# Kernel tuning notes

Hardware: AMD Instinct MI355X
Metric: run time of the kernel (lower is better)

The kernel has to match this reference:

```python
import jax, jax.numpy as jnp
import numpy as np

DEPTH = 6
INPUT_DIM = 512
HIDDEN = [128, 64]
OUT_DIM = 8
BATCH = 8192
NUM_LEAVES = 2 ** DEPTH            # 64
NUM_INTERNAL = 2 ** DEPTH - 1      # 63 routing Dense(1, sigmoid) nodes


def setup_inputs() -> dict:
    key = jax.random.key(0)
    ks = jax.random.split(key, 9)
    s = lambda fan_in: 1.0 / np.sqrt(fan_in)
    return {
        "x": jax.random.normal(ks[0], (BATCH, INPUT_DIM), dtype=jnp.float32),
        # routers: one Dense(input_dim -> 1) per internal node
        "router_W": jax.random.normal(ks[1], (NUM_INTERNAL, INPUT_DIM), dtype=jnp.float32) * s(INPUT_DIM),
        "router_b": jnp.zeros((NUM_INTERNAL,), dtype=jnp.float32),
        # leaf MLPs: Dense(512->128, relu) -> Dense(128->64, relu) -> Dense(64->8, linear), one per leaf
        "W1": jax.random.normal(ks[2], (NUM_LEAVES, INPUT_DIM, HIDDEN[0]), dtype=jnp.float32) * s(INPUT_DIM),
        "b1": jnp.zeros((NUM_LEAVES, HIDDEN[0]), dtype=jnp.float32),
        "W2": jax.random.normal(ks[3], (NUM_LEAVES, HIDDEN[0], HIDDEN[1]), dtype=jnp.float32) * s(HIDDEN[0]),
        "b2": jnp.zeros((NUM_LEAVES, HIDDEN[1]), dtype=jnp.float32),
        "W3": jax.random.normal(ks[4], (NUM_LEAVES, HIDDEN[1], OUT_DIM), dtype=jnp.float32) * s(HIDDEN[1]),
        "b3": jnp.zeros((NUM_LEAVES, OUT_DIM), dtype=jnp.float32),
    }


def reference(x, router_W, router_b, W1, b1, W2, b2, W3, b3):
    B = x.shape[0]
    depth = int(np.log2(router_W.shape[0] + 1))
    # All routing probabilities in one fused GEMM: [B, num_internal]
    route = jax.nn.sigmoid(jnp.einsum('bi,ni->bn', x, router_W) + router_b)
    # Soft routing down the tree: interleave left/right child probabilities per level.
    p = jnp.ones((B, 1), dtype=x.dtype)
    offset = 0
    for level in range(depth):  # small fixed loop over tree levels
        n = 2 ** level
        d = route[:, offset:offset + n]              # P(go left) at each node in level
        p = jnp.stack([p * d, p * (1.0 - d)], axis=-1).reshape(B, 2 * n)
        offset += n
    # p: [B, num_leaves] leaf arrival probabilities (sums to 1 per row)
    # Leaf experts as batched (grouped) GEMMs over the leaf axis l.
    h = jax.nn.relu(jnp.einsum('bi,lih->blh', x, W1) + b1)   # [B, L, 128]
    h = jax.nn.relu(jnp.einsum('blh,lhk->blk', h, W2) + b2)  # [B, L, 64]
    pred = jnp.einsum('blk,lko->blo', h, W3) + b3            # [B, L, out] (linear output act)
    # Weighted mixture over leaves.
    return jnp.einsum('bl,blo->bo', p, pred)                 # [B, out]
```

## Files before the change

### kernel.cpp

```cpp
#include <hip/hip_runtime.h>
#include <hip/hip_bf16.h>


typedef _Float16 f16;
typedef _Float16 f16x8 __attribute__((ext_vector_type(8)));
typedef float    f32x4 __attribute__((ext_vector_type(4)));
typedef float    f32x16 __attribute__((ext_vector_type(16)));

#define MFMA16(a,b,c) __builtin_amdgcn_mfma_f32_16x16x32_f16((a),(b),(c),0,0,0)
#define MFMA32(a,b,c) __builtin_amdgcn_mfma_f32_32x32x16_f16((a),(b),(c),0,0,0)

typedef const __attribute__((address_space(1))) void gv_t;
typedef __attribute__((address_space(3))) void lv_t;
__device__ __forceinline__ void cp16(const void* g, char* lds_dst) {
  __builtin_amdgcn_global_load_lds((gv_t*)g, (lv_t*)lds_dst, 16, 0, 0);
}

#define WS_XH    0u
#define WS_W1F   8388608u
#define WS_W2F   16777216u
#define WS_W3F   17825792u
#define WS_RWF   17956864u
#define WS_NEED  18022400u

#define L_X   0
#define L_H1  32768
#define L_H2  50176
#define L_P   59392
#define L_TOT 63488

__global__ __launch_bounds__(256) void prep_all(
    const float* __restrict__ x, const float* __restrict__ rW,
    const float* __restrict__ W1, const float* __restrict__ W2,
    const float* __restrict__ W3,
    f16* __restrict__ xh, f16* __restrict__ w1f, f16* __restrict__ w2f,
    f16* __restrict__ w3f, f16* __restrict__ rwf, float* __restrict__ out) {
  const int bid = blockIdx.x, t = threadIdx.x;
  if (bid < 512) {
    const int l = bid >> 3, kc = bid & 7;
    const int lane = t & 63;
#pragma unroll
    for (int p = 0; p < 4; ++p) {
      int c = p * 4 + (t >> 6);
      int ng = c >> 2, ksl = c & 3;
      int n = ng * 32 + (lane & 31);
      int k0 = kc * 64 + ksl * 16 + (lane >> 5) * 8;
      const float* src = W1 + ((size_t)l * 512 + k0) * 128 + n;
      f16x8 h;
#pragma unroll
      for (int j = 0; j < 8; ++j) h[j] = (f16)src[(size_t)j * 128];
      *(f16x8*)(w1f + ((size_t)((l * 4 + ng) * 32 + kc * 4 + ksl) * 64 + lane) * 8) = h;
    }
  } else if (bid < 768) {
    size_t base = (size_t)(bid - 512) * 16384;
#pragma unroll
    for (int i = 0; i < 8; ++i) {
      size_t idx = base + ((size_t)t + i * 256) * 8;
      float4 a = *(const float4*)(x + idx);
      float4 b = *(const float4*)(x + idx + 4);
      f16x8 h = {(f16)a.x,(f16)a.y,(f16)a.z,(f16)a.w,(f16)b.x,(f16)b.y,(f16)b.z,(f16)b.w};
      *(f16x8*)(xh + idx) = h;
    }
  } else if (bid < 832) {
    const int l = bid - 768;
    const int lane = t & 63;
#pragma unroll
    for (int p = 0; p < 4; ++p) {
      int c = p * 4 + (t >> 6);
      int nb = c >> 2, ks = c & 3;
      int n = nb * 16 + (lane & 15);
      int k0 = ks * 32 + (lane >> 4) * 8;
      const float* src = W2 + (size_t)l * 8192 + (size_t)k0 * 64 + n;
      f16x8 h;
#pragma unroll
      for (int j = 0; j < 8; ++j) h[j] = (f16)src[(size_t)j * 64];
      *(f16x8*)(w2f + ((size_t)((l * 4 + nb) * 4 + ks) * 64 + lane) * 8) = h;
    }
    if (t < 128) {
      int ks = t >> 6, lane2 = t & 63;
      int n = lane2 & 15;
      int k0 = ks * 32 + (lane2 >> 4) * 8;
      f16x8 h;
#pragma unroll
      for (int j = 0; j < 8; ++j)
        h[j] = (n < 8) ? (f16)W3[((size_t)l * 64 + k0 + j) * 8 + n] : (f16)0.f;
      *(f16x8*)(w3f + ((size_t)(l * 2 + ks) * 64 + lane2) * 8) = h;
    }
  } else {
    int c = (bid - 832) * 4 + (t >> 6);
    int ngr = c >> 5, ks = c & 31;
    int lane = t & 63;
    int n = ngr * 32 + (lane & 31);
    int k0 = ks * 16 + (lane >> 5) * 8;
    f16x8 h;
#pragma unroll
    for (int j = 0; j < 8; ++j)
      h[j] = (n < 63) ? (f16)rW[(size_t)n * 512 + k0 + j] : (f16)0.f;
    *(f16x8*)(rwf + ((size_t)c * 64 + lane) * 8) = h;
    size_t o0 = ((size_t)(bid - 832) * 256 + t) * 16;
    float4 z = {0.f, 0.f, 0.f, 0.f};
#pragma unroll
    for (int i = 0; i < 4; ++i) *(float4*)(out + o0 + i * 4) = z;
  }
}

__global__ __launch_bounds__(256, 2) void fused_tree(
    const f16* __restrict__ xh, const f16* __restrict__ w1f,
    const f16* __restrict__ w2f, const f16* __restrict__ w3f,
    const f16* __restrict__ rwf, const float* __restrict__ rb,
    const float* __restrict__ b1, const float* __restrict__ b2,
    const float* __restrict__ b3, float* __restrict__ out) {
  __shared__ char smem[L_TOT];
  f16*   x_lds   = (f16*)(smem + L_X);
  f16*   h1_lds  = (f16*)(smem + L_H1);
  float* route_s = (float*)(smem + L_H1);
  f16*   h2_lds  = (f16*)(smem + L_H2);
  float* p_lds   = (float*)(smem + L_P);

  const int t = threadIdx.x;
  const int w = t >> 6, L = t & 63;
  const int l16 = L & 15, quad = L >> 4;
  const int r31 = L & 31, kp = L >> 5;

  const int bid = blockIdx.x;
  const int r8 = bid & 7;
  const int lg0 = (r8 >> 1) * 16;
  const int btp = (bid >> 3) * 2 + (r8 & 1);
  const int b0 = btp * 64;

#pragma unroll
  for (int j = 0; j < 8; ++j) {
    int r = w * 8 + j;
    int u = (L & 56) | ((L & 7) ^ (r & 7));
    cp16(xh + (size_t)(b0 + 32 + r) * 512 + u * 8, smem + r * 1024);
  }
  f16x8 a0[32];
#pragma unroll
  for (int ks = 0; ks < 32; ++ks)
    a0[ks] = *(const f16x8*)(xh + (size_t)(b0 + r31) * 512 + ks * 16 + kp * 8);
  __syncthreads();

  {
    const int btr = w >> 1, ngr = w & 1;
    f32x16 accr;
#pragma unroll
    for (int i = 0; i < 16; ++i) accr[i] = 0.f;
    const f16* rbase = rwf + (size_t)(ngr * 32) * 512 + (size_t)L * 8;
#pragma unroll
    for (int ks = 0; ks < 32; ++ks) {
      f16x8 B = *(const f16x8*)(rbase + (size_t)ks * 512);
      f16x8 A;
      if (btr == 0) A = a0[ks];
      else {
        int u = ks * 2 + kp;
        A = *(const f16x8*)(x_lds + r31 * 512 + ((u & 56) | ((u & 7) ^ (r31 & 7))) * 8);
      }
      accr = MFMA32(A, B, accr);
    }
    int node = ngr * 32 + r31;
    float rbv = (node < 63) ? rb[node] : 0.f;
#pragma unroll
    for (int reg = 0; reg < 16; ++reg) {
      int rr = btr * 32 + (reg & 3) + 8 * (reg >> 2) + 4 * kp;
      route_s[rr * 68 + node] = 1.f / (1.f + __expf(-(accr[reg] + rbv)));
    }
  }
  __syncthreads();
  {
    int row = t >> 2, j0 = t & 3;
#pragma unroll
    for (int i = 0; i < 4; ++i) {
      int l = lg0 + j0 * 4 + i;
      float pr = 1.f;
#pragma unroll
      for (int lev = 0; lev < 6; ++lev) {
        int node = (1 << lev) - 1 + (l >> (6 - lev));
        float d = route_s[row * 68 + node];
        pr *= ((l >> (5 - lev)) & 1) ? (1.f - d) : d;
      }
      p_lds[row * 16 + j0 * 4 + i] = pr;
    }
  }
  __syncthreads();

  const f16* w1base = w1f + ((size_t)(lg0 * 4 + w) * 32) * 512 + (size_t)L * 8;
  f16x8 bq[2][4];
#pragma unroll
  for (int s = 0; s < 4; ++s) bq[0][s] = *(const f16x8*)(w1base + (size_t)s * 512);

  f32x4 acc_out = {0.f, 0.f, 0.f, 0.f};
  const int mt = w >> 1, nt2 = w & 1;
  const int n1 = w * 32 + r31;

#pragma unroll 1
  for (int li = 0; li < 16; ++li) {
    const int l = lg0 + li;
    const size_t leafoff = (size_t)li * 65536;

    f32x16 acc1r, acc1l;
#pragma unroll
    for (int i = 0; i < 16; ++i) { acc1r[i] = 0.f; acc1l[i] = 0.f; }

#pragma unroll
    for (int q = 0; q < 8; ++q) {
      f16x8 A1[4];
#pragma unroll
      for (int s = 0; s < 4; ++s) {
        int u = (q * 4 + s) * 2 + kp;
        A1[s] = *(const f16x8*)(x_lds + r31 * 512 + ((u & 56) | ((u & 7) ^ (r31 & 7))) * 8);
      }
      size_t nxt = (q < 7) ? (leafoff + (size_t)(q + 1) * 2048)
                           : ((li < 15) ? (leafoff + 65536) : (leafoff + 7 * 2048));
#pragma unroll
      for (int s = 0; s < 4; ++s)
        bq[(q + 1) & 1][s] = *(const f16x8*)(w1base + nxt + (size_t)s * 512);
      __builtin_amdgcn_s_setprio(1);
#pragma unroll
      for (int s = 0; s < 4; ++s)
        acc1r = MFMA32(a0[q * 4 + s], bq[q & 1][s], acc1r);
#pragma unroll
      for (int s = 0; s < 4; ++s)
        acc1l = MFMA32(A1[s], bq[q & 1][s], acc1l);
      __builtin_amdgcn_s_setprio(0);
    }

    f16x8 bw2[2][4];
#pragma unroll
    for (int n16 = 0; n16 < 2; ++n16)
#pragma unroll
      for (int ks = 0; ks < 4; ++ks)
        bw2[n16][ks] = *(const f16x8*)(w2f + ((size_t)((l * 4 + nt2 * 2 + n16) * 4 + ks) * 64 + L) * 8);
    f16x8 bw3[2];
#pragma unroll
    for (int ks = 0; ks < 2; ++ks)
      bw3[ks] = *(const f16x8*)(w3f + ((size_t)(l * 2 + ks) * 64 + L) * 8);

    const float bias1 = b1[l * 128 + n1];

#pragma unroll
    for (int reg = 0; reg < 16; ++reg) {
      int rr = (reg & 3) + 8 * (reg >> 2) + 4 * kp;
      float v0 = acc1r[reg] + bias1;
      float v1 = acc1l[reg] + bias1;
      h1_lds[rr * 136 + n1] = (f16)(v0 > 0.f ? v0 : 0.f);
      h1_lds[(rr + 32) * 136 + n1] = (f16)(v1 > 0.f ? v1 : 0.f);
    }
    __syncthreads();

#define GEMM2_BT(btv)                                                          \
    {                                                                          \
      f32x4 acc2[2] = {{0.f,0.f,0.f,0.f},{0.f,0.f,0.f,0.f}};                   \
      _Pragma("unroll")                                                        \
      for (int ks = 0; ks < 4; ++ks) {                                         \
        f16x8 A = *(const f16x8*)(h1_lds + ((btv) * 32 + mt * 16 + l16) * 136 + ks * 32 + quad * 8); \
        _Pragma("unroll")                                                      \
        for (int n16 = 0; n16 < 2; ++n16) acc2[n16] = MFMA16(A, bw2[n16][ks], acc2[n16]); \
      }                                                                        \
      _Pragma("unroll")                                                        \
      for (int n16 = 0; n16 < 2; ++n16) {                                      \
        int n2 = nt2 * 32 + n16 * 16 + l16;                                    \
        float bias2 = b2[l * 64 + n2];                                         \
        _Pragma("unroll")                                                      \
        for (int rg = 0; rg < 4; ++rg) {                                       \
          int r2 = mt * 16 + quad * 4 + rg;                                    \
          float v = acc2[n16][rg] + bias2;                                     \
          v = v > 0.f ? v : 0.f;                                               \
          h2_lds[((btv) * 32 + r2) * 72 + n2] = (f16)(v * p_lds[((btv) * 32 + r2) * 16 + li]); \
        }                                                                      \
      }                                                                        \
    }

    GEMM2_BT(0)
    GEMM2_BT(1)
#undef GEMM2_BT
    __syncthreads();

#pragma unroll
    for (int ks = 0; ks < 2; ++ks) {
      f16x8 A = *(const f16x8*)(h2_lds + (w * 16 + l16) * 72 + ks * 32 + quad * 8);
      acc_out = MFMA16(A, bw3[ks], acc_out);
    }
  }

  if (l16 < 8) {
    float b3v[16];
#pragma unroll
    for (int li2 = 0; li2 < 16; ++li2) b3v[li2] = b3[(lg0 + li2) * 8 + l16];
#pragma unroll
    for (int rg = 0; rg < 4; ++rg) {
      int rloc = w * 16 + quad * 4 + rg;
      float v = acc_out[rg];
#pragma unroll
      for (int li2 = 0; li2 < 16; ++li2) v += p_lds[rloc * 16 + li2] * b3v[li2];
      atomicAdd(out + (size_t)(b0 + rloc) * 8 + l16, v);
    }
  }
}

extern "C" void kernel_launch(void* const* d_in, const int* in_sizes, int n_in,
                              void* d_out, int out_size, void* d_ws, size_t ws_size,
                              hipStream_t stream) {
  const float* x  = (const float*)d_in[0];
  const float* rW = (const float*)d_in[1];
  const float* rb = (const float*)d_in[2];
  const float* W1 = (const float*)d_in[3];
  const float* b1 = (const float*)d_in[4];
  const float* W2 = (const float*)d_in[5];
  const float* b2 = (const float*)d_in[6];
  const float* W3 = (const float*)d_in[7];
  const float* b3 = (const float*)d_in[8];
  float* out = (float*)d_out;

  if (ws_size < WS_NEED) return;

  char* ws = (char*)d_ws;
  f16* xh  = (f16*)(ws + WS_XH);
  f16* w1f = (f16*)(ws + WS_W1F);
  f16* w2f = (f16*)(ws + WS_W2F);
  f16* w3f = (f16*)(ws + WS_W3F);
  f16* rwf = (f16*)(ws + WS_RWF);

  prep_all<<<848, 256, 0, stream>>>(x, rW, W1, W2, W3, xh, w1f, w2f, w3f, rwf, out);
  fused_tree<<<512, 256, 0, stream>>>(xh, w1f, w2f, w3f, rwf, rb, b1, b2, b3, out);
}
```

Before: 190.6 us.

## Halve batch tile to 32 rows per block, dropping x LDS staging

Each block now handles 32 batch rows instead of 64, so the second half of x no longer needs staging in LDS. The x-in-LDS path is removed, which cuts shared memory per block from about 62 KB to 15 KB. The grid doubles to 1024 blocks and launch bounds are raised to 4 blocks per CU for more parallelism and occupancy. The cost is that each W1/W2/W3 weight fetch is now reused over half as many rows, so weight traffic doubles, the output partials split across two waves, and there are twice as many atomics.

```diff
diff --git a/kernel.cpp b/kernel.cpp
--- a/kernel.cpp
+++ b/kernel.cpp
@@ -9,12 +9,6 @@
 
 #define MFMA16(a,b,c) __builtin_amdgcn_mfma_f32_16x16x32_f16((a),(b),(c),0,0,0)
 #define MFMA32(a,b,c) __builtin_amdgcn_mfma_f32_32x32x16_f16((a),(b),(c),0,0,0)
-
-typedef const __attribute__((address_space(1))) void gv_t;
-typedef __attribute__((address_space(3))) void lv_t;
-__device__ __forceinline__ void cp16(const void* g, char* lds_dst) {
-  __builtin_amdgcn_global_load_lds((gv_t*)g, (lv_t*)lds_dst, 16, 0, 0);
-}
 
 #define WS_XH    0u
 #define WS_W1F   8388608u
@@ -23,11 +17,10 @@
 #define WS_RWF   17956864u
 #define WS_NEED  18022400u
 
-#define L_X   0
-#define L_H1  32768
-#define L_H2  50176
-#define L_P   59392
-#define L_TOT 63488
+#define L_H1  0
+#define L_H2  8704
+#define L_P   13312
+#define L_TOT 15360
 
 __global__ __launch_bounds__(256) void prep_all(
     const float* __restrict__ x, const float* __restrict__ rW,
@@ -104,14 +97,13 @@
   }
 }
 
-__global__ __launch_bounds__(256, 2) void fused_tree(
+__global__ __launch_bounds__(256, 4) void fused_tree(
     const f16* __restrict__ xh, const f16* __restrict__ w1f,
     const f16* __restrict__ w2f, const f16* __restrict__ w3f,
     const f16* __restrict__ rwf, const float* __restrict__ rb,
     const float* __restrict__ b1, const float* __restrict__ b2,
     const float* __restrict__ b3, float* __restrict__ out) {
   __shared__ char smem[L_TOT];
-  f16*   x_lds   = (f16*)(smem + L_X);
   f16*   h1_lds  = (f16*)(smem + L_H1);
   float* route_s = (float*)(smem + L_H1);
   f16*   h2_lds  = (f16*)(smem + L_H2);
@@ -126,22 +118,15 @@
   const int r8 = bid & 7;
   const int lg0 = (r8 >> 1) * 16;
   const int btp = (bid >> 3) * 2 + (r8 & 1);
-  const int b0 = btp * 64;
-
-#pragma unroll
-  for (int j = 0; j < 8; ++j) {
-    int r = w * 8 + j;
-    int u = (L & 56) | ((L & 7) ^ (r & 7));
-    cp16(xh + (size_t)(b0 + 32 + r) * 512 + u * 8, smem + r * 1024);
-  }
+  const int b0 = btp * 32;
+
   f16x8 a0[32];
 #pragma unroll
   for (int ks = 0; ks < 32; ++ks)
     a0[ks] = *(const f16x8*)(xh + (size_t)(b0 + r31) * 512 + ks * 16 + kp * 8);
-  __syncthreads();
-
-  {
-    const int btr = w >> 1, ngr = w & 1;
+
+  if (w < 2) {
+    const int ngr = w;
     f32x16 accr;
 #pragma unroll
     for (int i = 0; i < 16; ++i) accr[i] = 0.f;
@@ -149,24 +134,18 @@
 #pragma unroll
     for (int ks = 0; ks < 32; ++ks) {
       f16x8 B = *(const f16x8*)(rbase + (size_t)ks * 512);
-      f16x8 A;
-      if (btr == 0) A = a0[ks];
-      else {
-        int u = ks * 2 + kp;
-        A = *(const f16x8*)(x_lds + r31 * 512 + ((u & 56) | ((u & 7) ^ (r31 & 7))) * 8);
-      }
-      accr = MFMA32(A, B, accr);
+      accr = MFMA32(a0[ks], B, accr);
     }
     int node = ngr * 32 + r31;
     float rbv = (node < 63) ? rb[node] : 0.f;
 #pragma unroll
     for (int reg = 0; reg < 16; ++reg) {
-      int rr = btr * 32 + (reg & 3) + 8 * (reg >> 2) + 4 * kp;
+      int rr = (reg & 3) + 8 * (reg >> 2) + 4 * kp;
       route_s[rr * 68 + node] = 1.f / (1.f + __expf(-(accr[reg] + rbv)));
     }
   }
   __syncthreads();
-  {
+  if (t < 128) {
     int row = t >> 2, j0 = t & 3;
 #pragma unroll
     for (int i = 0; i < 4; ++i) {
@@ -183,32 +162,28 @@
   }
   __syncthreads();
 
-  const f16* w1base = w1f + ((size_t)(lg0 * 4 + w) * 32) * 512 + (size_t)L * 8;
+  const int ng = w;
+  const f16* w1base = w1f + ((size_t)(lg0 * 4 + ng) * 32) * 512 + (size_t)L * 8;
   f16x8 bq[2][4];
 #pragma unroll
   for (int s = 0; s < 4; ++s) bq[0][s] = *(const f16x8*)(w1base + (size_t)s * 512);
 
   f32x4 acc_out = {0.f, 0.f, 0.f, 0.f};
   const int mt = w >> 1, nt2 = w & 1;
-  const int n1 = w * 32 + r31;
+  const int rb3 = w >> 1, ks3 = w & 1;
+  const int n1 = ng * 32 + r31;
 
 #pragma unroll 1
   for (int li = 0; li < 16; ++li) {
     const int l = lg0 + li;
     const size_t leafoff = (size_t)li * 65536;
 
-    f32x16 acc1r, acc1l;
-#pragma unroll
-    for (int i = 0; i < 16; ++i) { acc1r[i] = 0.f; acc1l[i] = 0.f; }
+    f32x16 acc1;
+#pragma unroll
+    for (int i = 0; i < 16; ++i) acc1[i] = 0.f;
 
 #pragma unroll
     for (int q = 0; q < 8; ++q) {
-      f16x8 A1[4];
-#pragma unroll
-      for (int s = 0; s < 4; ++s) {
-        int u = (q * 4 + s) * 2 + kp;
-        A1[s] = *(const f16x8*)(x_lds + r31 * 512 + ((u & 56) | ((u & 7) ^ (r31 & 7))) * 8);
-      }
       size_t nxt = (q < 7) ? (leafoff + (size_t)(q + 1) * 2048)
                            : ((li < 15) ? (leafoff + 65536) : (leafoff + 7 * 2048));
 #pragma unroll
@@ -217,10 +192,7 @@
       __builtin_amdgcn_s_setprio(1);
 #pragma unroll
       for (int s = 0; s < 4; ++s)
-        acc1r = MFMA32(a0[q * 4 + s], bq[q & 1][s], acc1r);
-#pragma unroll
-      for (int s = 0; s < 4; ++s)
-        acc1l = MFMA32(A1[s], bq[q & 1][s], acc1l);
+        acc1 = MFMA32(a0[q * 4 + s], bq[q & 1][s], acc1);
       __builtin_amdgcn_s_setprio(0);
     }
 
@@ -230,55 +202,44 @@
 #pragma unroll
       for (int ks = 0; ks < 4; ++ks)
         bw2[n16][ks] = *(const f16x8*)(w2f + ((size_t)((l * 4 + nt2 * 2 + n16) * 4 + ks) * 64 + L) * 8);
-    f16x8 bw3[2];
-#pragma unroll
-    for (int ks = 0; ks < 2; ++ks)
-      bw3[ks] = *(const f16x8*)(w3f + ((size_t)(l * 2 + ks) * 64 + L) * 8);
+    f16x8 bw3 = *(const f16x8*)(w3f + ((size_t)(l * 2 + ks3) * 64 + L) * 8);
 
     const float bias1 = b1[l * 128 + n1];
 
 #pragma unroll
     for (int reg = 0; reg < 16; ++reg) {
       int rr = (reg & 3) + 8 * (reg >> 2) + 4 * kp;
-      float v0 = acc1r[reg] + bias1;
-      float v1 = acc1l[reg] + bias1;
-      h1_lds[rr * 136 + n1] = (f16)(v0 > 0.f ? v0 : 0.f);
-      h1_lds[(rr + 32) * 136 + n1] = (f16)(v1 > 0.f ? v1 : 0.f);
+      float v = acc1[reg] + bias1;
+      h1_lds[rr * 136 + n1] = (f16)(v > 0.f ? v : 0.f);
     }
     __syncthreads();
 
-#define GEMM2_BT(btv)                                                          \
-    {                                                                          \
-      f32x4 acc2[2] = {{0.f,0.f,0.f,0.f},{0.f,0.f,0.f,0.f}};                   \
-      _Pragma("unroll")                                                        \
-      for (int ks = 0; ks < 4; ++ks) {                                         \
-        f16x8 A = *(const f16x8*)(h1_lds + ((btv) * 32 + mt * 16 + l16) * 136 + ks * 32 + quad * 8); \
-        _Pragma("unroll")                                                      \
-        for (int n16 = 0; n16 < 2; ++n16) acc2[n16] = MFMA16(A, bw2[n16][ks], acc2[n16]); \
-      }                                                                        \
-      _Pragma("unroll")                                                        \
-      for (int n16 = 0; n16 < 2; ++n16) {                                      \
-        int n2 = nt2 * 32 + n16 * 16 + l16;                                    \
-        float bias2 = b2[l * 64 + n2];                                         \
-        _Pragma("unroll")                                                      \
-        for (int rg = 0; rg < 4; ++rg) {                                       \
-          int r2 = mt * 16 + quad * 4 + rg;                                    \
-          float v = acc2[n16][rg] + bias2;                                     \
-          v = v > 0.f ? v : 0.f;                                               \
-          h2_lds[((btv) * 32 + r2) * 72 + n2] = (f16)(v * p_lds[((btv) * 32 + r2) * 16 + li]); \
-        }                                                                      \
-      }                                                                        \
-    }
-
-    GEMM2_BT(0)
-    GEMM2_BT(1)
-#undef GEMM2_BT
+    {
+      f32x4 acc2[2] = {{0.f,0.f,0.f,0.f},{0.f,0.f,0.f,0.f}};
+#pragma unroll
+      for (int ks = 0; ks < 4; ++ks) {
+        f16x8 A = *(const f16x8*)(h1_lds + (mt * 16 + l16) * 136 + ks * 32 + quad * 8);
+#pragma unroll
+        for (int n16 = 0; n16 < 2; ++n16) acc2[n16] = MFMA16(A, bw2[n16][ks], acc2[n16]);
+      }
+#pragma unroll
+      for (int n16 = 0; n16 < 2; ++n16) {
+        int n2 = nt2 * 32 + n16 * 16 + l16;
+        float bias2 = b2[l * 64 + n2];
+#pragma unroll
+        for (int rg = 0; rg < 4; ++rg) {
+          int r2 = mt * 16 + quad * 4 + rg;
+          float v = acc2[n16][rg] + bias2;
+          v = v > 0.f ? v : 0.f;
+          h2_lds[r2 * 72 + n2] = (f16)(v * p_lds[r2 * 16 + li]);
+        }
+      }
+    }
     __syncthreads();
 
-#pragma unroll
-    for (int ks = 0; ks < 2; ++ks) {
-      f16x8 A = *(const f16x8*)(h2_lds + (w * 16 + l16) * 72 + ks * 32 + quad * 8);
-      acc_out = MFMA16(A, bw3[ks], acc_out);
+    {
+      f16x8 A = *(const f16x8*)(h2_lds + (rb3 * 16 + l16) * 72 + ks3 * 32 + quad * 8);
+      acc_out = MFMA16(A, bw3, acc_out);
     }
   }
 
@@ -288,10 +249,12 @@
     for (int li2 = 0; li2 < 16; ++li2) b3v[li2] = b3[(lg0 + li2) * 8 + l16];
 #pragma unroll
     for (int rg = 0; rg < 4; ++rg) {
-      int rloc = w * 16 + quad * 4 + rg;
+      int rloc = rb3 * 16 + quad * 4 + rg;
       float v = acc_out[rg];
-#pragma unroll
-      for (int li2 = 0; li2 < 16; ++li2) v += p_lds[rloc * 16 + li2] * b3v[li2];
+      if (ks3 == 0) {
+#pragma unroll
+        for (int li2 = 0; li2 < 16; ++li2) v += p_lds[rloc * 16 + li2] * b3v[li2];
+      }
       atomicAdd(out + (size_t)(b0 + rloc) * 8 + l16, v);
     }
   }
@@ -321,5 +284,5 @@
   f16* rwf = (f16*)(ws + WS_RWF);
 
   prep_all<<<848, 256, 0, stream>>>(x, rW, W1, W2, W3, xh, w1f, w2f, w3f, rwf, out);
-  fused_tree<<<512, 256, 0, stream>>>(xh, w1f, w2f, w3f, rwf, rb, b1, b2, b3, out);
+  fused_tree<<<1024, 256, 0, stream>>>(xh, w1f, w2f, w3f, rwf, rb, b1, b2, b3, out);
 }
```

Result: slower. 415.5 us (+118.0%).
